# Kernel tuning notes

Hardware: AMD Instinct MI355X
Metric: run time of the kernel (lower is better)

## Reference

```python
import jax, jax.numpy as jnp
import numpy as np

N = 50000      # nodes
E = 800000     # edges (before self loops)
F_IN = 128
HID = 32
HEADS = 4
C = 64         # num_classes
SLOPE = 0.2    # LeakyReLU negative slope (PyG GATConv default)


def setup_inputs() -> dict:
    key = jax.random.key(0)
    ks = jax.random.split(key, 16)
    def nrm(k, shape, scale=0.1):
        return jax.random.normal(k, shape, jnp.float32) * scale
    x = jax.random.normal(ks[0], (N, F_IN), jnp.float32)
    edge_index = jax.random.randint(ks[1], (2, E), 0, N, jnp.int32)
    # layer 1: F_IN -> HID per head, concat -> HEADS*HID
    w1 = nrm(ks[2], (F_IN, HEADS * HID)); as1 = nrm(ks[3], (HEADS, HID)); ad1 = nrm(ks[4], (HEADS, HID)); b1 = nrm(ks[5], (HEADS * HID,))
    # layer 2: HEADS*HID -> HID per head, concat
    w2 = nrm(ks[6], (HEADS * HID, HEADS * HID)); as2 = nrm(ks[7], (HEADS, HID)); ad2 = nrm(ks[8], (HEADS, HID)); b2 = nrm(ks[9], (HEADS * HID,))
    # layer 3: HEADS*HID -> C, single head, no concat (mean)
    w3 = nrm(ks[10], (HEADS * HID, C)); as3 = nrm(ks[11], (1, C)); ad3 = nrm(ks[12], (1, C)); b3 = nrm(ks[13], (C,))
    return {"x": x, "edge_index": edge_index,
            "w1": w1, "as1": as1, "ad1": ad1, "b1": b1,
            "w2": w2, "as2": as2, "ad2": ad2, "b2": b2,
            "w3": w3, "as3": as3, "ad3": ad3, "b3": b3}


def gat_conv(x, src, dst, W, a_src, a_dst, bias, heads, oc, concat):
    n = x.shape[0]
    h = (x @ W).reshape(n, heads, oc)                       # [N,H,F]
    al_s = jnp.einsum('nhf,hf->nh', h, a_src)               # [N,H]
    al_d = jnp.einsum('nhf,hf->nh', h, a_dst)
    e = jax.nn.leaky_relu(al_s[src] + al_d[dst], SLOPE)     # [E,H]
    # segment softmax over incoming edges per destination node
    m = jax.ops.segment_max(e, dst, num_segments=n)
    e = jnp.exp(e - m[dst])
    denom = jax.ops.segment_sum(e, dst, num_segments=n)
    alpha = e / denom[dst]                                  # [E,H]
    out = jax.ops.segment_sum(h[src] * alpha[:, :, None], dst, num_segments=n)  # [N,H,F]
    out = out.reshape(n, heads * oc) if concat else out.mean(axis=1)
    return out + bias


def reference(x, edge_index, w1, as1, ad1, b1, w2, as2, ad2, b2, w3, as3, ad3, b3):
    n = x.shape[0]
    loops = jnp.arange(n, dtype=edge_index.dtype)
    src = jnp.concatenate([edge_index[0], loops])           # add self loops (PyG default)
    dst = jnp.concatenate([edge_index[1], loops])
    h = gat_conv(x, src, dst, w1, as1, ad1, b1, HEADS, HID, True)
    h = jax.nn.relu(h)                                      # dropout is identity in eval
    h = gat_conv(h, src, dst, w2, as2, ad2, b2, HEADS, HID, True)
    h = jax.nn.relu(h)
    h = gat_conv(h, src, dst, w3, as3, ad3, b3, 1, C, False)
    return jax.nn.log_softmax(h, axis=1)
```

## Files before the change

### kernel.cpp

```cpp
#include <hip/hip_runtime.h>
#include <hip/hip_bf16.h>
#include <math.h>

#define SLOPE 0.2f
typedef unsigned int uint_t;
typedef unsigned short ushort_t;
typedef __attribute__((ext_vector_type(8))) short short8;
typedef __attribute__((ext_vector_type(4))) float f32x4;

static __device__ __forceinline__ float lrelu(float v) { return v > 0.f ? v : SLOPE * v; }
static __device__ __forceinline__ ushort_t f2b(float f) {
  uint_t u = __float_as_uint(f);
  u += 0x7fffu + ((u >> 16) & 1u);
  return (ushort_t)(u >> 16);
}
static __device__ __forceinline__ float2 b2x2(uint_t u) {
  union { uint_t u; __hip_bfloat162 b; } cv;
  cv.u = u;
  return __bfloat1622float2(cv.b);
}


__device__ __forceinline__ void hist_body(const int* __restrict__ ei, int* __restrict__ ts,
                                          int E, int N, int NB, int NBUCK, int b) {
  __shared__ int h[256];
  int tid = threadIdx.x;
  h[tid] = 0;
  __syncthreads();
  int ET = E + N;
  int base = b * 4096;
#pragma unroll
  for (int j = 0; j < 16; ++j) {
    int i = base + j * 256 + tid;
    if (i < ET) {
      int d = (i < E) ? ei[E + i] : (i - E);
      atomicAdd(&h[d >> 8], 1);
    }
  }
  __syncthreads();
  if (tid < NBUCK) ts[tid * NB + b] = h[tid];
}

__global__ __launch_bounds__(256) void scan1(int* __restrict__ a, int* __restrict__ bsum, int L) {
  int tid = threadIdx.x;
  int base = blockIdx.x * 1024 + tid * 4;
  int c0 = (base + 0 < L) ? a[base + 0] : 0;
  int c1 = (base + 1 < L) ? a[base + 1] : 0;
  int c2 = (base + 2 < L) ? a[base + 2] : 0;
  int c3 = (base + 3 < L) ? a[base + 3] : 0;
  int s = c0 + c1 + c2 + c3;
  int lane = tid & 63, wid = tid >> 6;
  int pre = s;
#pragma unroll
  for (int off = 1; off < 64; off <<= 1) {
    int t = __shfl_up(pre, off);
    if (lane >= off) pre += t;
  }
  __shared__ int wsum[4];
  if (lane == 63) wsum[wid] = pre;
  __syncthreads();
  int woff = 0;
#pragma unroll
  for (int w = 0; w < 4; ++w) woff += (w < wid) ? wsum[w] : 0;
  int excl = woff + pre - s;
  if (base + 0 < L) a[base + 0] = excl;
  if (base + 1 < L) a[base + 1] = excl + c0;
  if (base + 2 < L) a[base + 2] = excl + c0 + c1;
  if (base + 3 < L) a[base + 3] = excl + c0 + c1 + c2;
  if (tid == 255) bsum[blockIdx.x] = wsum[0] + wsum[1] + wsum[2] + wsum[3];
}

__global__ __launch_bounds__(1024) void scan2(int* __restrict__ bsum, int nb) {
  __shared__ int sh[1024];
  int tid = threadIdx.x;
  int v = (tid < nb) ? bsum[tid] : 0;
  sh[tid] = v;
  __syncthreads();
  for (int off = 1; off < 1024; off <<= 1) {
    int add = (tid >= off) ? sh[tid - off] : 0;
    __syncthreads();
    sh[tid] += add;
    __syncthreads();
  }
  if (tid < nb) bsum[tid] = sh[tid] - v;
}

__global__ __launch_bounds__(256) void part_kernel(const int* __restrict__ ei,
                                                   const int* __restrict__ ts,
                                                   const int* __restrict__ bsum,
                                                   uint_t* __restrict__ tmp,
                                                   int E, int N, int NB, int NBUCK) {
  __shared__ int bin[256];
  int tid = threadIdx.x, b = blockIdx.x;
  if (tid < NBUCK) {
    int idx = tid * NB + b;
    bin[tid] = ts[idx] + bsum[idx >> 10];
  }
  __syncthreads();
  int ET = E + N;
  int base = b * 4096;
#pragma unroll
  for (int j = 0; j < 16; ++j) {
    int i = base + j * 256 + tid;
    if (i < ET) {
      int s, d;
      if (i < E) { s = ei[i]; d = ei[E + i]; } else { s = i - E; d = i - E; }
      int pos = atomicAdd(&bin[d >> 8], 1);
      tmp[pos] = ((uint_t)d << 16) | (uint_t)s;
    }
  }
}

__global__ __launch_bounds__(256) void bucket_kernel(const uint_t* __restrict__ tmp,
                                                     const int* __restrict__ ts,
                                                     const int* __restrict__ bsum,
                                                     int* __restrict__ rowptr,
                                                     int* __restrict__ esrc,
                                                     int N, int NB, int NBUCK, int ET) {
  __shared__ int h[256], pref[256], rank[256];
  __shared__ int wsum[4];
  int tid = threadIdx.x, d = blockIdx.x;
  int i0 = d * NB;
  int start = ts[i0] + bsum[i0 >> 10];
  int end = ET;
  if (d != NBUCK - 1) {
    int i1 = (d + 1) * NB;
    end = ts[i1] + bsum[i1 >> 10];
  }
  h[tid] = 0; rank[tid] = 0;
  __syncthreads();
  for (int i = start + tid; i < end; i += 256)
    atomicAdd(&h[(tmp[i] >> 16) & 255], 1);
  __syncthreads();
  int v = h[tid];
  int lane = tid & 63, wid = tid >> 6;
  int inc = v;
#pragma unroll
  for (int off = 1; off < 64; off <<= 1) {
    int t = __shfl_up(inc, off);
    if (lane >= off) inc += t;
  }
  if (lane == 63) wsum[wid] = inc;
  __syncthreads();
  int woff = 0;
#pragma unroll
  for (int w = 0; w < 4; ++w) woff += (w < wid) ? wsum[w] : 0;
  pref[tid] = woff + inc - v;
  __syncthreads();
  int idx = d * 256 + tid;
  if (idx <= N) rowptr[idx] = start + pref[tid];
  for (int i = start + tid; i < end; i += 256) {
    uint_t v2 = tmp[i];
    int low = (v2 >> 16) & 255;
    int r = atomicAdd(&rank[low], 1);
    esrc[start + pref[low] + r] = (int)(v2 & 0xffffu);
  }
}


__device__ __forceinline__ void gemm1_body(const float* __restrict__ X,
                                           const float* __restrict__ W,
                                           ushort_t* __restrict__ H,
                                           const float* __restrict__ a_s,
                                           const float* __restrict__ a_d,
                                           float* __restrict__ als,
                                           float* __restrict__ ald,
                                           int N, int bid) {
  const int K = 128;
  const int OC = 128;
  const int CT = 32;
  const int RPT = 8;
  __shared__ float xs[K][68];
  int tid = threadIdx.x;
  long row0 = (long)bid * 64;
#pragma unroll
  for (int i = 0; i < 8; ++i) {
    int flat = i * 256 + tid;
    int r = flat & 63, kc = flat >> 6;
    long row = row0 + r;
    long rr = row < N ? row : (long)(N - 1);
    float4 xv = *(const float4*)(X + rr * K + kc * 4);
    xs[kc * 4 + 0][r] = xv.x;
    xs[kc * 4 + 1][r] = xv.y;
    xs[kc * 4 + 2][r] = xv.z;
    xs[kc * 4 + 3][r] = xv.w;
  }
  __syncthreads();
  int ct = tid % CT;
  int rg = tid / CT;
  int c0 = ct * 4;
  int r0 = rg * RPT;
  float acc[RPT][4];
#pragma unroll
  for (int i = 0; i < RPT; ++i)
    for (int j = 0; j < 4; ++j) acc[i][j] = 0.f;
#pragma unroll 4
  for (int k = 0; k < K; ++k) {
    float4 wv = *(const float4*)(W + (long)k * OC + c0);
    const float4* xr = (const float4*)(&xs[k][r0]);
#pragma unroll
    for (int i4 = 0; i4 < RPT / 4; ++i4) {
      float4 xv = xr[i4];
      float xa[4] = {xv.x, xv.y, xv.z, xv.w};
#pragma unroll
      for (int j = 0; j < 4; ++j) {
        int i = i4 * 4 + j;
        acc[i][0] = fmaf(xa[j], wv.x, acc[i][0]);
        acc[i][1] = fmaf(xa[j], wv.y, acc[i][1]);
        acc[i][2] = fmaf(xa[j], wv.z, acc[i][2]);
        acc[i][3] = fmaf(xa[j], wv.w, acc[i][3]);
      }
    }
  }
#pragma unroll
  for (int i = 0; i < RPT; ++i) {
    long row = row0 + r0 + i;
    if (row < N) {
      ushort4 o = {f2b(acc[i][0]), f2b(acc[i][1]), f2b(acc[i][2]), f2b(acc[i][3])};
      *(ushort4*)(H + row * OC + c0) = o;
    }
  }
  float4 sv = *(const float4*)(a_s + c0);
  float4 dv = *(const float4*)(a_d + c0);
#pragma unroll
  for (int i = 0; i < RPT; ++i) {
    float ps = acc[i][0] * sv.x + acc[i][1] * sv.y + acc[i][2] * sv.z + acc[i][3] * sv.w;
    float pd = acc[i][0] * dv.x + acc[i][1] * dv.y + acc[i][2] * dv.z + acc[i][3] * dv.w;
#pragma unroll
    for (int off = 1; off <= 4; off <<= 1) {
      ps += __shfl_xor(ps, off);
      pd += __shfl_xor(pd, off);
    }
    long row = row0 + r0 + i;
    if ((ct & 7) == 0 && row < N) {
      int head = c0 >> 5;
      als[row * 4 + head] = ps;
      ald[row * 4 + head] = pd;
    }
  }
}

__device__ __forceinline__ void wprep_body(const float* __restrict__ w2,
                                           const float* __restrict__ w3,
                                           ushort_t* __restrict__ wt2,
                                           ushort_t* __restrict__ wt3, int b) {
  int tid = threadIdx.x;
#pragma unroll
  for (int j = 0; j < 32; ++j) {
    int idx = b * 8192 + j * 256 + tid;
    if (idx < 16384) {
      int c = idx & 127, k = idx >> 7;
      wt2[c * 128 + k] = f2b(w2[idx]);
    } else if (idx < 24576) {
      int i2 = idx - 16384;
      int c = i2 & 63, k = i2 >> 6;
      wt3[c * 128 + k] = f2b(w3[i2]);
    }
  }
}

__global__ __launch_bounds__(256) void k_gemm1_hist(const float* __restrict__ X,
    const float* __restrict__ W, ushort_t* __restrict__ H,
    const float* __restrict__ a_s, const float* __restrict__ a_d,
    float* __restrict__ als, float* __restrict__ ald, int N,
    const int* __restrict__ ei, int* __restrict__ ts, int E, int NB, int NBUCK,
    const float* __restrict__ w2, const float* __restrict__ w3,
    ushort_t* __restrict__ wt2, ushort_t* __restrict__ wt3,
    int gemmBlocks) {
  int bid = blockIdx.x;
  if (bid < gemmBlocks) gemm1_body(X, W, H, a_s, a_d, als, ald, N, bid);
  else if (bid < gemmBlocks + NB) hist_body(ei, ts, E, N, NB, NBUCK, bid - gemmBlocks);
  else wprep_body(w2, w3, wt2, wt3, bid - gemmBlocks - NB);
}


template<int OC>
__global__ __launch_bounds__(256) void mfma_gemm(const ushort_t* __restrict__ X,
    const ushort_t* __restrict__ WT, ushort_t* __restrict__ H,
    const float* __restrict__ a_s, const float* __restrict__ a_d,
    float* __restrict__ als, float* __restrict__ ald, int N) {
  const int K = 128;
  const int P = 136;
  const int MT = OC / 16;
  __shared__ ushort_t xs[64 * P];
  int tid = threadIdx.x;
  long row0 = (long)blockIdx.x * 64;
#pragma unroll
  for (int i = 0; i < 4; ++i) {
    int flat = i * 256 + tid;
    int r = flat & 63, kc = flat >> 6;
    long row = row0 + r;
    long rr = row < N ? row : (long)(N - 1);
    uint4 v = *(const uint4*)(X + rr * K + kc * 8);
    *(uint4*)(xs + r * P + kc * 8) = v;
  }
  __syncthreads();
  int wave = tid >> 6, lane = tid & 63;
  int n = lane & 15, q = lane >> 4;
  int wrow = wave * 16 + n;
  f32x4 acc[MT];
#pragma unroll
  for (int t = 0; t < MT; ++t) acc[t] = (f32x4){0.f, 0.f, 0.f, 0.f};
#pragma unroll
  for (int kk = 0; kk < 4; ++kk) {
    short8 bfrag = *(const short8*)(xs + wrow * P + kk * 32 + q * 8);
#pragma unroll
    for (int t = 0; t < MT; ++t) {
      short8 afrag = *(const short8*)(WT + (t * 16 + n) * K + kk * 32 + q * 8);
      acc[t] = __builtin_amdgcn_mfma_f32_16x16x32_bf16(afrag, bfrag, acc[t], 0, 0, 0);
    }
  }
  long grow = row0 + wrow;
  bool valid = grow < N;
  float ps[4] = {0.f, 0.f, 0.f, 0.f};
  float pd[4] = {0.f, 0.f, 0.f, 0.f};
#pragma unroll
  for (int t = 0; t < MT; ++t) {
    int fb = t * 16 + q * 4;
    if (valid) {
      uint_t lo = (uint_t)f2b(acc[t][0]) | ((uint_t)f2b(acc[t][1]) << 16);
      uint_t hi = (uint_t)f2b(acc[t][2]) | ((uint_t)f2b(acc[t][3]) << 16);
      uint2 pk = {lo, hi};
      *(uint2*)(H + grow * OC + fb) = pk;
    }
    float4 sv = *(const float4*)(a_s + fb);
    float4 dv = *(const float4*)(a_d + fb);
    int hidx = (OC == 128) ? (t >> 1) : 0;
    ps[hidx] += acc[t][0] * sv.x + acc[t][1] * sv.y + acc[t][2] * sv.z + acc[t][3] * sv.w;
    pd[hidx] += acc[t][0] * dv.x + acc[t][1] * dv.y + acc[t][2] * dv.z + acc[t][3] * dv.w;
  }
  const int NH = (OC == 128) ? 4 : 1;
#pragma unroll
  for (int h = 0; h < NH; ++h) {
    ps[h] += __shfl_xor(ps[h], 16); ps[h] += __shfl_xor(ps[h], 32);
    pd[h] += __shfl_xor(pd[h], 16); pd[h] += __shfl_xor(pd[h], 32);
  }
  if (q == 0 && valid) {
    if (OC == 128) {
      float4 s4 = {ps[0], ps[1], ps[2], ps[3]};
      float4 d4 = {pd[0], pd[1], pd[2], pd[3]};
      *(float4*)(als + grow * 4) = s4;
      *(float4*)(ald + grow * 4) = d4;
    } else {
      als[grow] = ps[0];
      ald[grow] = pd[0];
    }
  }
}


__global__ __launch_bounds__(256) void gat_agg128(const ushort_t* __restrict__ h,
    const float* __restrict__ als, const float* __restrict__ ald,
    const int* __restrict__ rowptr, const int* __restrict__ esrc,
    const float* __restrict__ bias, ushort_t* __restrict__ out, int N) {
  int tid = threadIdx.x;
  int n = blockIdx.x * 8 + (tid >> 5);
  int l = tid & 31;
  int slot = l >> 3, sl = l & 7, hd = sl >> 1;
  if (n >= N) return;
  int beg = rowptr[n], end = rowptr[n + 1];
  float aldv = ald[(long)n * 4 + hd];
  float den = 0.f;
  float acc[16];
#pragma unroll
  for (int j = 0; j < 16; ++j) acc[j] = 0.f;
  for (int e = beg + slot; e < end; e += 4) {
    int s = esrc[e];
    float p = __expf(lrelu(als[(long)s * 4 + hd] + aldv));
    den += p;
    const ushort_t* hp = h + (long)s * 128 + sl * 16;
    uint4 v0 = *(const uint4*)(hp);
    uint4 v1 = *(const uint4*)(hp + 8);
    uint_t vv[8] = {v0.x, v0.y, v0.z, v0.w, v1.x, v1.y, v1.z, v1.w};
#pragma unroll
    for (int j = 0; j < 8; ++j) {
      float2 f = b2x2(vv[j]);
      acc[2 * j + 0] = fmaf(p, f.x, acc[2 * j + 0]);
      acc[2 * j + 1] = fmaf(p, f.y, acc[2 * j + 1]);
    }
  }
  den += __shfl_xor(den, 8); den += __shfl_xor(den, 16);
#pragma unroll
  for (int j = 0; j < 16; ++j) {
    acc[j] += __shfl_xor(acc[j], 8);
    acc[j] += __shfl_xor(acc[j], 16);
  }
  if (slot == 0) {
    float inv = 1.f / den;
    uint_t pk[8];
#pragma unroll
    for (int j = 0; j < 8; ++j) {
      float v0 = fmaxf(fmaf(acc[2 * j + 0], inv, bias[sl * 16 + 2 * j + 0]), 0.f);
      float v1 = fmaxf(fmaf(acc[2 * j + 1], inv, bias[sl * 16 + 2 * j + 1]), 0.f);
      pk[j] = (uint_t)f2b(v0) | ((uint_t)f2b(v1) << 16);
    }
    uint4 o0 = {pk[0], pk[1], pk[2], pk[3]};
    uint4 o1 = {pk[4], pk[5], pk[6], pk[7]};
    *(uint4*)(out + (long)n * 128 + sl * 16 + 0) = o0;
    *(uint4*)(out + (long)n * 128 + sl * 16 + 8) = o1;
  }
}

__global__ __launch_bounds__(256) void gat_agg64_lsm(const ushort_t* __restrict__ h,
    const float* __restrict__ als, const float* __restrict__ ald,
    const int* __restrict__ rowptr, const int* __restrict__ esrc,
    const float* __restrict__ bias, float* __restrict__ out, int N) {
  int tid = threadIdx.x;
  int n = blockIdx.x * 8 + (tid >> 5);
  int l = tid & 31;
  int slot = l >> 2, sl = l & 3;
  if (n >= N) return;
  int beg = rowptr[n], end = rowptr[n + 1];
  float aldv = ald[n];
  float den = 0.f;
  float acc[16];
#pragma unroll
  for (int j = 0; j < 16; ++j) acc[j] = 0.f;
  for (int e = beg + slot; e < end; e += 8) {
    int s = esrc[e];
    float p = __expf(lrelu(als[s] + aldv));
    den += p;
    const ushort_t* hp = h + (long)s * 64 + sl * 16;
    uint4 v0 = *(const uint4*)(hp);
    uint4 v1 = *(const uint4*)(hp + 8);
    uint_t vv[8] = {v0.x, v0.y, v0.z, v0.w, v1.x, v1.y, v1.z, v1.w};
#pragma unroll
    for (int j = 0; j < 8; ++j) {
      float2 f = b2x2(vv[j]);
      acc[2 * j + 0] = fmaf(p, f.x, acc[2 * j + 0]);
      acc[2 * j + 1] = fmaf(p, f.y, acc[2 * j + 1]);
    }
  }
  den += __shfl_xor(den, 4); den += __shfl_xor(den, 8); den += __shfl_xor(den, 16);
#pragma unroll
  for (int j = 0; j < 16; ++j) {
    acc[j] += __shfl_xor(acc[j], 4);
    acc[j] += __shfl_xor(acc[j], 8);
    acc[j] += __shfl_xor(acc[j], 16);
  }
  if (slot == 0) {
    float inv = 1.f / den;
    float v[16];
#pragma unroll
    for (int j = 0; j < 16; ++j) v[j] = fmaf(acc[j], inv, bias[sl * 16 + j]);
    float lm = v[0];
#pragma unroll
    for (int j = 1; j < 16; ++j) lm = fmaxf(lm, v[j]);
    lm = fmaxf(lm, __shfl_xor(lm, 1));
    lm = fmaxf(lm, __shfl_xor(lm, 2));
    float es = 0.f;
#pragma unroll
    for (int j = 0; j < 16; ++j) es += __expf(v[j] - lm);
    es += __shfl_xor(es, 1);
    es += __shfl_xor(es, 2);
    float lse = lm + __logf(es);
    float* op = out + (long)n * 64 + sl * 16;
#pragma unroll
    for (int qq = 0; qq < 4; ++qq) {
      float4 o = {v[4 * qq + 0] - lse, v[4 * qq + 1] - lse, v[4 * qq + 2] - lse, v[4 * qq + 3] - lse};
      *(float4*)(op + 4 * qq) = o;
    }
  }
}


extern "C" void kernel_launch(void* const* d_in, const int* in_sizes, int n_in,
                              void* d_out, int out_size, void* d_ws, size_t ws_size,
                              hipStream_t stream) {
  const float* x   = (const float*)d_in[0];
  const int*   ei  = (const int*)d_in[1];
  const float* w1  = (const float*)d_in[2];
  const float* as1 = (const float*)d_in[3];
  const float* ad1 = (const float*)d_in[4];
  const float* b1  = (const float*)d_in[5];
  const float* w2  = (const float*)d_in[6];
  const float* as2 = (const float*)d_in[7];
  const float* ad2 = (const float*)d_in[8];
  const float* b2  = (const float*)d_in[9];
  const float* w3  = (const float*)d_in[10];
  const float* as3 = (const float*)d_in[11];
  const float* ad3 = (const float*)d_in[12];
  const float* b3  = (const float*)d_in[13];
  float* out = (float*)d_out;

  const int N = in_sizes[0] / 128;
  const int E = in_sizes[1] / 2;
  const int ET = E + N;

  const int NB = (ET + 4095) / 4096;
  const int NBUCK = (N + 255) >> 8;
  const int SL = NBUCK * NB;
  const int nsb = (SL + 1023) / 1024;

  char* ws = (char*)d_ws;
  size_t off = 0;
  auto alloc = [&](size_t bytes) -> void* {
    void* p = ws + off;
    off += (bytes + 255) & ~(size_t)255;
    return p;
  };
  ushort_t* bufA = (ushort_t*)alloc((size_t)N * 128 * 2);
  ushort_t* bufB = (ushort_t*)alloc((size_t)N * 128 * 2);
  float* als   = (float*)alloc((size_t)N * 4 * 4);
  float* ald   = (float*)alloc((size_t)N * 4 * 4);
  int* ts      = (int*)alloc((size_t)SL * 4);
  int* bsum    = (int*)alloc((size_t)1024 * 4);
  uint_t* tmp  = (uint_t*)alloc((size_t)ET * 4);
  int* rowptr  = (int*)alloc((size_t)(N + 1) * 4);
  int* esrc    = (int*)alloc((size_t)ET * 4);
  ushort_t* wt2 = (ushort_t*)alloc((size_t)128 * 128 * 2);
  ushort_t* wt3 = (ushort_t*)alloc((size_t)64 * 128 * 2);

  const int ggrid = (N + 63) / 64;
  const int aggrid = (N + 7) / 8;

  k_gemm1_hist<<<ggrid + NB + 3, 256, 0, stream>>>(x, w1, bufA, as1, ad1, als, ald, N,
                                                   ei, ts, E, NB, NBUCK,
                                                   w2, w3, wt2, wt3, ggrid);
  scan1<<<nsb, 256, 0, stream>>>(ts, bsum, SL);
  scan2<<<1, 1024, 0, stream>>>(bsum, nsb);
  part_kernel<<<NB, 256, 0, stream>>>(ei, ts, bsum, tmp, E, N, NB, NBUCK);
  bucket_kernel<<<NBUCK, 256, 0, stream>>>(tmp, ts, bsum, rowptr, esrc, N, NB, NBUCK, ET);

  gat_agg128<<<aggrid, 256, 0, stream>>>(bufA, als, ald, rowptr, esrc, b1, bufB, N);

  mfma_gemm<128><<<ggrid, 256, 0, stream>>>(bufB, wt2, bufA, as2, ad2, als, ald, N);
  gat_agg128<<<aggrid, 256, 0, stream>>>(bufA, als, ald, rowptr, esrc, b2, bufB, N);

  mfma_gemm<64><<<ggrid, 256, 0, stream>>>(bufB, wt3, bufA, as3, ad3, als, ald, N);
  gat_agg64_lsm<<<aggrid, 256, 0, stream>>>(bufA, als, ald, rowptr, esrc, b3, out, N);
}
```

Measured before the change: 286.4 us.

## Move layer-1 GEMM to bf16 MFMA path and fuse scan1 into it

Replaces the fp32 FMA layer-1 GEMM with the existing bf16 MFMA GEMM body. A new pre-kernel converts x to bf16 and transposes w1 alongside the histogram and other weight prep. scan1 is folded into the GEMM launch as extra blocks, so the total launch count stays the same. The trade-off is an extra bf16 copy of x written and re-read, plus reduced precision for layer 1.

After: 293.7 us. 1.03x slower.

```diff
diff --git a/kernel.cpp b/kernel.cpp
--- a/kernel.cpp
+++ b/kernel.cpp
@@ -41,9 +41,10 @@
   if (tid < NBUCK) ts[tid * NB + b] = h[tid];
 }
 
-__global__ __launch_bounds__(256) void scan1(int* __restrict__ a, int* __restrict__ bsum, int L) {
-  int tid = threadIdx.x;
-  int base = blockIdx.x * 1024 + tid * 4;
+__device__ __forceinline__ void scan1_body(int* __restrict__ a, int* __restrict__ bsum,
+                                           int L, int bid) {
+  int tid = threadIdx.x;
+  int base = bid * 1024 + tid * 4;
   int c0 = (base + 0 < L) ? a[base + 0] : 0;
   int c1 = (base + 1 < L) ? a[base + 1] : 0;
   int c2 = (base + 2 < L) ? a[base + 2] : 0;
@@ -67,7 +68,7 @@
   if (base + 1 < L) a[base + 1] = excl + c0;
   if (base + 2 < L) a[base + 2] = excl + c0 + c1;
   if (base + 3 < L) a[base + 3] = excl + c0 + c1 + c2;
-  if (tid == 255) bsum[blockIdx.x] = wsum[0] + wsum[1] + wsum[2] + wsum[3];
+  if (tid == 255) bsum[bid] = wsum[0] + wsum[1] + wsum[2] + wsum[3];
 }
 
 __global__ __launch_bounds__(1024) void scan2(int* __restrict__ bsum, int nb) {
@@ -158,90 +159,24 @@
 }
 
 
-__device__ __forceinline__ void gemm1_body(const float* __restrict__ X,
-                                           const float* __restrict__ W,
-                                           ushort_t* __restrict__ H,
-                                           const float* __restrict__ a_s,
-                                           const float* __restrict__ a_d,
-                                           float* __restrict__ als,
-                                           float* __restrict__ ald,
-                                           int N, int bid) {
-  const int K = 128;
-  const int OC = 128;
-  const int CT = 32;
-  const int RPT = 8;
-  __shared__ float xs[K][68];
-  int tid = threadIdx.x;
-  long row0 = (long)bid * 64;
-#pragma unroll
-  for (int i = 0; i < 8; ++i) {
-    int flat = i * 256 + tid;
-    int r = flat & 63, kc = flat >> 6;
-    long row = row0 + r;
-    long rr = row < N ? row : (long)(N - 1);
-    float4 xv = *(const float4*)(X + rr * K + kc * 4);
-    xs[kc * 4 + 0][r] = xv.x;
-    xs[kc * 4 + 1][r] = xv.y;
-    xs[kc * 4 + 2][r] = xv.z;
-    xs[kc * 4 + 3][r] = xv.w;
-  }
-  __syncthreads();
-  int ct = tid % CT;
-  int rg = tid / CT;
-  int c0 = ct * 4;
-  int r0 = rg * RPT;
-  float acc[RPT][4];
-#pragma unroll
-  for (int i = 0; i < RPT; ++i)
-    for (int j = 0; j < 4; ++j) acc[i][j] = 0.f;
-#pragma unroll 4
-  for (int k = 0; k < K; ++k) {
-    float4 wv = *(const float4*)(W + (long)k * OC + c0);
-    const float4* xr = (const float4*)(&xs[k][r0]);
-#pragma unroll
-    for (int i4 = 0; i4 < RPT / 4; ++i4) {
-      float4 xv = xr[i4];
-      float xa[4] = {xv.x, xv.y, xv.z, xv.w};
-#pragma unroll
-      for (int j = 0; j < 4; ++j) {
-        int i = i4 * 4 + j;
-        acc[i][0] = fmaf(xa[j], wv.x, acc[i][0]);
-        acc[i][1] = fmaf(xa[j], wv.y, acc[i][1]);
-        acc[i][2] = fmaf(xa[j], wv.z, acc[i][2]);
-        acc[i][3] = fmaf(xa[j], wv.w, acc[i][3]);
-      }
-    }
-  }
-#pragma unroll
-  for (int i = 0; i < RPT; ++i) {
-    long row = row0 + r0 + i;
-    if (row < N) {
-      ushort4 o = {f2b(acc[i][0]), f2b(acc[i][1]), f2b(acc[i][2]), f2b(acc[i][3])};
-      *(ushort4*)(H + row * OC + c0) = o;
-    }
-  }
-  float4 sv = *(const float4*)(a_s + c0);
-  float4 dv = *(const float4*)(a_d + c0);
-#pragma unroll
-  for (int i = 0; i < RPT; ++i) {
-    float ps = acc[i][0] * sv.x + acc[i][1] * sv.y + acc[i][2] * sv.z + acc[i][3] * sv.w;
-    float pd = acc[i][0] * dv.x + acc[i][1] * dv.y + acc[i][2] * dv.z + acc[i][3] * dv.w;
-#pragma unroll
-    for (int off = 1; off <= 4; off <<= 1) {
-      ps += __shfl_xor(ps, off);
-      pd += __shfl_xor(pd, off);
-    }
-    long row = row0 + r0 + i;
-    if ((ct & 7) == 0 && row < N) {
-      int head = c0 >> 5;
-      als[row * 4 + head] = ps;
-      ald[row * 4 + head] = pd;
-    }
-  }
-}
-
-__device__ __forceinline__ void wprep_body(const float* __restrict__ w2,
+__device__ __forceinline__ void conv_body(const float* __restrict__ x,
+                                          ushort_t* __restrict__ bx, int total8, int b) {
+  int g = b * 256 + threadIdx.x;
+  if (g >= total8) return;
+  const float4* xp = (const float4*)(x + (long)g * 8);
+  float4 v0 = xp[0], v1 = xp[1];
+  uint_t p0 = (uint_t)f2b(v0.x) | ((uint_t)f2b(v0.y) << 16);
+  uint_t p1 = (uint_t)f2b(v0.z) | ((uint_t)f2b(v0.w) << 16);
+  uint_t p2 = (uint_t)f2b(v1.x) | ((uint_t)f2b(v1.y) << 16);
+  uint_t p3 = (uint_t)f2b(v1.z) | ((uint_t)f2b(v1.w) << 16);
+  uint4 pk = {p0, p1, p2, p3};
+  *(uint4*)(bx + (long)g * 8) = pk;
+}
+
+__device__ __forceinline__ void wprep_body(const float* __restrict__ w1,
+                                           const float* __restrict__ w2,
                                            const float* __restrict__ w3,
+                                           ushort_t* __restrict__ wt1,
                                            ushort_t* __restrict__ wt2,
                                            ushort_t* __restrict__ wt3, int b) {
   int tid = threadIdx.x;
@@ -250,41 +185,50 @@
     int idx = b * 8192 + j * 256 + tid;
     if (idx < 16384) {
       int c = idx & 127, k = idx >> 7;
-      wt2[c * 128 + k] = f2b(w2[idx]);
-    } else if (idx < 24576) {
+      wt1[c * 128 + k] = f2b(w1[idx]);
+    } else if (idx < 32768) {
       int i2 = idx - 16384;
-      int c = i2 & 63, k = i2 >> 6;
-      wt3[c * 128 + k] = f2b(w3[i2]);
-    }
-  }
-}
-
-__global__ __launch_bounds__(256) void k_gemm1_hist(const float* __restrict__ X,
-    const float* __restrict__ W, ushort_t* __restrict__ H,
-    const float* __restrict__ a_s, const float* __restrict__ a_d,
-    float* __restrict__ als, float* __restrict__ ald, int N,
-    const int* __restrict__ ei, int* __restrict__ ts, int E, int NB, int NBUCK,
-    const float* __restrict__ w2, const float* __restrict__ w3,
-    ushort_t* __restrict__ wt2, ushort_t* __restrict__ wt3,
-    int gemmBlocks) {
+      int c = i2 & 127, k = i2 >> 7;
+      wt2[c * 128 + k] = f2b(w2[i2]);
+    } else if (idx < 40960) {
+      int i3 = idx - 32768;
+      int c = i3 & 63, k = i3 >> 6;
+      wt3[c * 128 + k] = f2b(w3[i3]);
+    }
+  }
+}
+
+__global__ __launch_bounds__(256) void k_pre(const int* __restrict__ ei, int* __restrict__ ts,
+                                             int E, int N, int NB, int NBUCK,
+                                             const float* __restrict__ w1,
+                                             const float* __restrict__ w2,
+                                             const float* __restrict__ w3,
+                                             ushort_t* __restrict__ wt1,
+                                             ushort_t* __restrict__ wt2,
+                                             ushort_t* __restrict__ wt3,
+                                             const float* __restrict__ x,
+                                             ushort_t* __restrict__ bx, int total8) {
   int bid = blockIdx.x;
-  if (bid < gemmBlocks) gemm1_body(X, W, H, a_s, a_d, als, ald, N, bid);
-  else if (bid < gemmBlocks + NB) hist_body(ei, ts, E, N, NB, NBUCK, bid - gemmBlocks);
-  else wprep_body(w2, w3, wt2, wt3, bid - gemmBlocks - NB);
+  if (bid < NB) hist_body(ei, ts, E, N, NB, NBUCK, bid);
+  else if (bid < NB + 5) wprep_body(w1, w2, w3, wt1, wt2, wt3, bid - NB);
+  else conv_body(x, bx, total8, bid - NB - 5);
 }
 
 
 template<int OC>
-__global__ __launch_bounds__(256) void mfma_gemm(const ushort_t* __restrict__ X,
-    const ushort_t* __restrict__ WT, ushort_t* __restrict__ H,
-    const float* __restrict__ a_s, const float* __restrict__ a_d,
-    float* __restrict__ als, float* __restrict__ ald, int N) {
+__device__ __forceinline__ void mfma_body(const ushort_t* __restrict__ X,
+                                          const ushort_t* __restrict__ WT,
+                                          ushort_t* __restrict__ H,
+                                          const float* __restrict__ a_s,
+                                          const float* __restrict__ a_d,
+                                          float* __restrict__ als,
+                                          float* __restrict__ ald, int N, int bid) {
   const int K = 128;
   const int P = 136;
   const int MT = OC / 16;
   __shared__ ushort_t xs[64 * P];
   int tid = threadIdx.x;
-  long row0 = (long)blockIdx.x * 64;
+  long row0 = (long)bid * 64;
 #pragma unroll
   for (int i = 0; i < 4; ++i) {
     int flat = i * 256 + tid;
@@ -346,6 +290,24 @@
       ald[grow] = pd[0];
     }
   }
+}
+
+template<int OC>
+__global__ __launch_bounds__(256) void mfma_gemm(const ushort_t* __restrict__ X,
+    const ushort_t* __restrict__ WT, ushort_t* __restrict__ H,
+    const float* __restrict__ a_s, const float* __restrict__ a_d,
+    float* __restrict__ als, float* __restrict__ ald, int N) {
+  mfma_body<OC>(X, WT, H, a_s, a_d, als, ald, N, blockIdx.x);
+}
+
+__global__ __launch_bounds__(256) void k_gemm1_scan1(const ushort_t* __restrict__ X,
+    const ushort_t* __restrict__ WT, ushort_t* __restrict__ H,
+    const float* __restrict__ a_s, const float* __restrict__ a_d,
+    float* __restrict__ als, float* __restrict__ ald, int N,
+    int* __restrict__ ts, int* __restrict__ bsum, int SL, int gemmBlocks) {
+  int bid = blockIdx.x;
+  if (bid < gemmBlocks) mfma_body<128>(X, WT, H, a_s, a_d, als, ald, N, bid);
+  else scan1_body(ts, bsum, SL, bid - gemmBlocks);
 }
 
 
@@ -491,6 +453,8 @@
   const int NBUCK = (N + 255) >> 8;
   const int SL = NBUCK * NB;
   const int nsb = (SL + 1023) / 1024;
+  const int total8 = N * 16;
+  const int cvB = (total8 + 255) / 256;
 
   char* ws = (char*)d_ws;
   size_t off = 0;
@@ -499,6 +463,7 @@
     off += (bytes + 255) & ~(size_t)255;
     return p;
   };
+  ushort_t* bufX = (ushort_t*)alloc((size_t)N * 128 * 2);
   ushort_t* bufA = (ushort_t*)alloc((size_t)N * 128 * 2);
   ushort_t* bufB = (ushort_t*)alloc((size_t)N * 128 * 2);
   float* als   = (float*)alloc((size_t)N * 4 * 4);
@@ -508,16 +473,17 @@
   uint_t* tmp  = (uint_t*)alloc((size_t)ET * 4);
   int* rowptr  = (int*)alloc((size_t)(N + 1) * 4);
   int* esrc    = (int*)alloc((size_t)ET * 4);
+  ushort_t* wt1 = (ushort_t*)alloc((size_t)128 * 128 * 2);
   ushort_t* wt2 = (ushort_t*)alloc((size_t)128 * 128 * 2);
   ushort_t* wt3 = (ushort_t*)alloc((size_t)64 * 128 * 2);
 
   const int ggrid = (N + 63) / 64;
   const int aggrid = (N + 7) / 8;
 
-  k_gemm1_hist<<<ggrid + NB + 3, 256, 0, stream>>>(x, w1, bufA, as1, ad1, als, ald, N,
-                                                   ei, ts, E, NB, NBUCK,
-                                                   w2, w3, wt2, wt3, ggrid);
-  scan1<<<nsb, 256, 0, stream>>>(ts, bsum, SL);
+  k_pre<<<NB + 5 + cvB, 256, 0, stream>>>(ei, ts, E, N, NB, NBUCK,
+                                          w1, w2, w3, wt1, wt2, wt3, x, bufX, total8);
+  k_gemm1_scan1<<<ggrid + nsb, 256, 0, stream>>>(bufX, wt1, bufA, as1, ad1, als, ald, N,
+                                                 ts, bsum, SL, ggrid);
   scan2<<<1, 1024, 0, stream>>>(bsum, nsb);
   part_kernel<<<NB, 256, 0, stream>>>(ei, ts, bsum, tmp, E, N, NB, NBUCK);
   bucket_kernel<<<NBUCK, 256, 0, stream>>>(tmp, ts, bsum, rowptr, esrc, N, NB, NBUCK, ET);
```
